# Performance work log

Hardware: AMD Instinct MI355X
Metric: run time of the kernel (lower is better)

Reference implementation:

```python
import jax, jax.numpy as jnp
import numpy as np

SEQ_LEN = 2_000_000
NUM_TAGS = 50


def setup_inputs() -> dict:
    key = jax.random.key(0)
    k1, k2, k3 = jax.random.split(key, 3)
    logits = jax.random.normal(k1, (SEQ_LEN, NUM_TAGS), dtype=jnp.float32)
    tags = jax.random.randint(k2, (SEQ_LEN,), 0, NUM_TAGS, dtype=jnp.int64)
    # learned parameter from __init__: transitions ~ randn(num_tags, num_tags)
    transitions = jax.random.normal(k3, (NUM_TAGS, NUM_TAGS), dtype=jnp.float32)
    return {"logits": logits, "tags": tags, "transitions": transitions}


def reference(logits, tags, transitions):
    # score = sum_i logits[i, tags[i]] + sum_{i>0} transitions[tags[i-1], tags[i]]
    # forward returns -score (negative path score, used as the loss)
    emit = jnp.take_along_axis(logits, tags[:, None], axis=1).sum()  # [S] gather -> scalar
    trans = transitions[tags[:-1], tags[1:]].sum()                   # [S-1] gather -> scalar
    return -(emit + trans)
```

## Files before the change

### kernel.cpp

```cpp
#include <hip/hip_runtime.h>
#include <stdint.h>


#define NUM_TAGS 50
#define TILE 128
#define LOG_CHUNKS 25
#define TAG_CHUNKS 3
#define OPS_PER_TILE (LOG_CHUNKS + TAG_CHUNKS)
#define GRID 512

typedef __attribute__((address_space(3))) uint32_t lds_u32_t;
typedef __attribute__((address_space(1))) uint32_t g_u32_t;

__device__ __forceinline__ void dma16(const void* gp, void* lds) {
    __builtin_amdgcn_global_load_lds((const g_u32_t*)(uintptr_t)gp,
        (lds_u32_t*)(uint32_t)(uintptr_t)lds, 16, 0, 0);
}
__device__ __forceinline__ void dma4(const void* gp, void* lds) {
    __builtin_amdgcn_global_load_lds((const g_u32_t*)(uintptr_t)gp,
        (lds_u32_t*)(uint32_t)(uintptr_t)lds, 4, 0, 0);
}

__global__ __launch_bounds__(64) void crf_score_kernel(
    const float* __restrict__ logits,
    const int*   __restrict__ tags,
    const float* __restrict__ trans,
    float* __restrict__ out,
    int n)
{
    __shared__ __align__(16) float s_log[2][TILE * NUM_TAGS];
    __shared__ __align__(16) int   s_tag[2][TAG_CHUNKS * 64];
    __shared__ __align__(16) float s_trans[NUM_TAGS * NUM_TAGS];

    const int lane = threadIdx.x;
    const long long nn = n;

    {
        const uint4* t4 = (const uint4*)trans;
        uint4* s4 = (uint4*)s_trans;
        for (int i = lane; i < (NUM_TAGS * NUM_TAGS) / 4; i += 64)
            s4[i] = t4[i];
    }

    const int ntiles = (int)((nn + TILE - 1) / TILE);
    const float* glim = logits + nn * NUM_TAGS;
    const int* tlim = tags + nn;

    auto stage = [&](int tile, int b) {
        const long long base = (long long)tile * TILE;
        const float* g = logits + base * NUM_TAGS;
        #pragma unroll
        for (int c = 0; c < LOG_CHUNKS; ++c) {
            const float* p = g + (c << 8) + (lane << 2);
            if (p + 4 > glim) p = glim - 4;
            dma16(p, &s_log[b][c << 8]);
        }
        const int* gt = tags + base;
        #pragma unroll
        for (int c = 0; c < TAG_CHUNKS; ++c) {
            const int* p = gt + (c << 6) + lane;
            if (p >= tlim) p = tags;
            dma4(p, &s_tag[b][c << 6]);
        }
    };

    float acc = 0.0f;
    const int tile0  = blockIdx.x;
    const int stride = gridDim.x;

    if (tile0 < ntiles) {
        stage(tile0, 0);
        if (tile0 + stride < ntiles) stage(tile0 + stride, 1);

        int b = 0;
        for (int t = tile0; t < ntiles; t += stride, b ^= 1) {
            if (t + stride < ntiles)
                asm volatile("s_waitcnt vmcnt(28)" ::: "memory");
            else
                asm volatile("s_waitcnt vmcnt(0)" ::: "memory");
            __builtin_amdgcn_sched_barrier(0);

            const long long base = (long long)t * TILE;
            const long long rem  = nn - base;
            const int rows = (rem < TILE) ? (int)rem : TILE;
            #pragma unroll
            for (int rh = 0; rh < 2; ++rh) {
                const int r = lane + (rh << 6);
                if (r < rows) {
                    const int tg = s_tag[b][r];
                    float v = s_log[b][r * NUM_TAGS + tg];
                    if (base + r + 1 < nn)
                        v += s_trans[tg * NUM_TAGS + s_tag[b][r + 1]];
                    acc += v;
                }
            }

            asm volatile("s_waitcnt lgkmcnt(0)" ::: "memory");
            __builtin_amdgcn_sched_barrier(0);

            const int tnext = t + 2 * stride;
            if (tnext < ntiles) stage(tnext, b);
        }
    }

    #pragma unroll
    for (int off = 32; off > 0; off >>= 1)
        acc += __shfl_down(acc, off, 64);
    if (lane == 0)
        atomicAdd(out, -acc);
}

extern "C" void kernel_launch(void* const* d_in, const int* in_sizes, int n_in,
                              void* d_out, int out_size, void* d_ws, size_t ws_size,
                              hipStream_t stream) {
    const float* logits = (const float*)d_in[0];
    const int*   tags   = (const int*)d_in[1];
    const float* trans  = (const float*)d_in[2];
    float* out = (float*)d_out;
    const int n = in_sizes[1];

    hipMemsetAsync(out, 0, sizeof(float), stream);

    const int ntiles = (n + TILE - 1) / TILE;
    const int grid = (ntiles < GRID) ? ntiles : GRID;
    crf_score_kernel<<<grid, 64, 0, stream>>>(logits, tags, trans, out, n);
}
```

Before: 523.9 us.

## Use two independent wave streams per block with smaller double-buffered tiles

Each 128-thread block now runs two waves, and each wave streams its own 64-row tiles through a private double-buffered LDS region. The transition table is shared across both waves. Tile loads split into 16-byte and 4-byte DMA pieces, and a fast path without clamping is used for interior tiles. The goal is more waves in flight and less LDS per tile, so more memory requests overlap. The cost is a shallower per-wave prefetch (16 ops instead of 28) and more loop overhead per row.

```diff
diff --git a/kernel.cpp b/kernel.cpp
--- a/kernel.cpp
+++ b/kernel.cpp
@@ -3,10 +3,13 @@
 
 
 #define NUM_TAGS 50
-#define TILE 128
-#define LOG_CHUNKS 25
-#define TAG_CHUNKS 3
-#define OPS_PER_TILE (LOG_CHUNKS + TAG_CHUNKS)
+#define TILE 64
+#define LOG16 12
+#define LOG4  2
+#define TAG4  2
+#define OPS (LOG16 + LOG4 + TAG4)
+#define THREADS 128
+#define WPB 2
 #define GRID 512
 
 typedef __attribute__((address_space(3))) uint32_t lds_u32_t;
@@ -21,61 +24,79 @@
         (lds_u32_t*)(uint32_t)(uintptr_t)lds, 4, 0, 0);
 }
 
-__global__ __launch_bounds__(64) void crf_score_kernel(
+__global__ __launch_bounds__(THREADS) void crf_score_kernel(
     const float* __restrict__ logits,
     const int*   __restrict__ tags,
     const float* __restrict__ trans,
     float* __restrict__ out,
     int n)
 {
-    __shared__ __align__(16) float s_log[2][TILE * NUM_TAGS];
-    __shared__ __align__(16) int   s_tag[2][TAG_CHUNKS * 64];
+    __shared__ __align__(16) float s_log[WPB][2][TILE * NUM_TAGS];
+    __shared__ __align__(16) int   s_tag[WPB][2][128];
     __shared__ __align__(16) float s_trans[NUM_TAGS * NUM_TAGS];
 
-    const int lane = threadIdx.x;
+    const int tid  = threadIdx.x;
+    const int lane = tid & 63;
+    const int w    = tid >> 6;
+
+    for (int i = tid; i < (NUM_TAGS * NUM_TAGS) / 4; i += THREADS)
+        ((uint4*)s_trans)[i] = ((const uint4*)trans)[i];
+    __syncthreads();
+
     const long long nn = n;
+    const int ntiles = (int)((nn + TILE - 1) / TILE);
+    const int stream = blockIdx.x * WPB + w;
+    const int stride = gridDim.x * WPB;
 
-    {
-        const uint4* t4 = (const uint4*)trans;
-        uint4* s4 = (uint4*)s_trans;
-        for (int i = lane; i < (NUM_TAGS * NUM_TAGS) / 4; i += 64)
-            s4[i] = t4[i];
-    }
-
-    const int ntiles = (int)((nn + TILE - 1) / TILE);
     const float* glim = logits + nn * NUM_TAGS;
-    const int* tlim = tags + nn;
+    const int*   tlim = tags + nn;
 
     auto stage = [&](int tile, int b) {
         const long long base = (long long)tile * TILE;
-        const float* g = logits + base * NUM_TAGS;
-        #pragma unroll
-        for (int c = 0; c < LOG_CHUNKS; ++c) {
-            const float* p = g + (c << 8) + (lane << 2);
-            if (p + 4 > glim) p = glim - 4;
-            dma16(p, &s_log[b][c << 8]);
-        }
-        const int* gt = tags + base;
-        #pragma unroll
-        for (int c = 0; c < TAG_CHUNKS; ++c) {
-            const int* p = gt + (c << 6) + lane;
-            if (p >= tlim) p = tags;
-            dma4(p, &s_tag[b][c << 6]);
+        const float* g  = logits + base * NUM_TAGS;
+        const int*   gt = tags + base;
+        if (base + TILE + 64 <= nn) {
+            #pragma unroll
+            for (int c = 0; c < LOG16; ++c)
+                dma16(g + (c << 8) + (lane << 2), &s_log[w][b][c << 8]);
+            #pragma unroll
+            for (int c = 0; c < LOG4; ++c)
+                dma4(g + (LOG16 << 8) + (c << 6) + lane,
+                     &s_log[w][b][(LOG16 << 8) + (c << 6)]);
+            #pragma unroll
+            for (int c = 0; c < TAG4; ++c)
+                dma4(gt + (c << 6) + lane, &s_tag[w][b][c << 6]);
+        } else {
+            #pragma unroll
+            for (int c = 0; c < LOG16; ++c) {
+                const float* p = g + (c << 8) + (lane << 2);
+                if (p + 4 > glim) p = glim - 4;
+                dma16(p, &s_log[w][b][c << 8]);
+            }
+            #pragma unroll
+            for (int c = 0; c < LOG4; ++c) {
+                const float* p = g + (LOG16 << 8) + (c << 6) + lane;
+                if (p + 1 > glim) p = glim - 1;
+                dma4(p, &s_log[w][b][(LOG16 << 8) + (c << 6)]);
+            }
+            #pragma unroll
+            for (int c = 0; c < TAG4; ++c) {
+                const int* p = gt + (c << 6) + lane;
+                if (p >= tlim) p = tags;
+                dma4(p, &s_tag[w][b][c << 6]);
+            }
         }
     };
 
     float acc = 0.0f;
-    const int tile0  = blockIdx.x;
-    const int stride = gridDim.x;
-
-    if (tile0 < ntiles) {
-        stage(tile0, 0);
-        if (tile0 + stride < ntiles) stage(tile0 + stride, 1);
+    if (stream < ntiles) {
+        stage(stream, 0);
+        if (stream + stride < ntiles) stage(stream + stride, 1);
 
         int b = 0;
-        for (int t = tile0; t < ntiles; t += stride, b ^= 1) {
+        for (int t = stream; t < ntiles; t += stride, b ^= 1) {
             if (t + stride < ntiles)
-                asm volatile("s_waitcnt vmcnt(28)" ::: "memory");
+                asm volatile("s_waitcnt vmcnt(16)" ::: "memory");
             else
                 asm volatile("s_waitcnt vmcnt(0)" ::: "memory");
             __builtin_amdgcn_sched_barrier(0);
@@ -83,23 +104,19 @@
             const long long base = (long long)t * TILE;
             const long long rem  = nn - base;
             const int rows = (rem < TILE) ? (int)rem : TILE;
-            #pragma unroll
-            for (int rh = 0; rh < 2; ++rh) {
-                const int r = lane + (rh << 6);
-                if (r < rows) {
-                    const int tg = s_tag[b][r];
-                    float v = s_log[b][r * NUM_TAGS + tg];
-                    if (base + r + 1 < nn)
-                        v += s_trans[tg * NUM_TAGS + s_tag[b][r + 1]];
-                    acc += v;
-                }
+            if (lane < rows) {
+                const int tg = s_tag[w][b][lane];
+                float v = s_log[w][b][lane * NUM_TAGS + tg];
+                if (base + lane + 1 < nn)
+                    v += s_trans[tg * NUM_TAGS + s_tag[w][b][lane + 1]];
+                acc += v;
             }
 
             asm volatile("s_waitcnt lgkmcnt(0)" ::: "memory");
             __builtin_amdgcn_sched_barrier(0);
 
-            const int tnext = t + 2 * stride;
-            if (tnext < ntiles) stage(tnext, b);
+            const int tn = t + 2 * stride;
+            if (tn < ntiles) stage(tn, b);
         }
     }
 
@@ -122,6 +139,7 @@
     hipMemsetAsync(out, 0, sizeof(float), stream);
 
     const int ntiles = (n + TILE - 1) / TILE;
-    const int grid = (ntiles < GRID) ? ntiles : GRID;
-    crf_score_kernel<<<grid, 64, 0, stream>>>(logits, tags, trans, out, n);
+    const int nstreams_needed = (ntiles + WPB - 1) / WPB;
+    const int grid = (nstreams_needed < GRID) ? nstreams_needed : GRID;
+    crf_score_kernel<<<grid, THREADS, 0, stream>>>(logits, tags, trans, out, n);
 }
```

Result: no change. 522.7 us (-0.2%).
